# Kernel optimization log

Measured on AMD Instinct MI355X. Metric: run time of the kernel, lower is better.

The kernel has to match this reference:

```python
import jax, jax.numpy as jnp
import numpy as np

N_NODES = 8192
N_EDGES = 49152
IN_F, HID, H1, H2, OUT_F = 128, 64, 64, 5, 32
N_BONDS = 64


def setup_inputs() -> dict:
    key = jax.random.key(0)
    ks = jax.random.split(key, 12)
    s = 0.05
    return {
        "x": jax.random.normal(ks[0], (N_NODES, IN_F), jnp.float32),
        "edge_index": jax.random.randint(ks[1], (2, N_EDGES), 0, N_NODES, jnp.int32),
        "lefts": jax.random.randint(ks[2], (N_BONDS,), 0, N_NODES, jnp.int32),
        "rights": jax.random.randint(ks[3], (N_BONDS,), 0, N_NODES, jnp.int32),
        "W1": jax.random.normal(ks[4], (H1 * HID, IN_F), jnp.float32) * s,
        "att_src1": jax.random.normal(ks[5], (H1, HID), jnp.float32) * s,
        "att_dst1": jax.random.normal(ks[6], (H1, HID), jnp.float32) * s,
        "b1": jnp.zeros((H1 * HID,), jnp.float32),
        "W2": jax.random.normal(ks[7], (H2 * OUT_F, H1 * HID), jnp.float32) * s,
        "att_src2": jax.random.normal(ks[8], (H2, OUT_F), jnp.float32) * s,
        "att_dst2": jax.random.normal(ks[9], (H2, OUT_F), jnp.float32) * s,
        "b2": jnp.zeros((OUT_F,), jnp.float32),
    }


def _gat_conv(x, src, dst, W, a_src, a_dst, b, concat):
    # x: [N, F_in]; W: [H*C, F_in]; a_src/a_dst: [H, C]
    N = x.shape[0]
    H, C = a_src.shape
    h = (x @ W.T).reshape(N, H, C)                    # [N, H, C]
    alpha_s = jnp.einsum("nhc,hc->nh", h, a_src)      # [N, H]
    alpha_d = jnp.einsum("nhc,hc->nh", h, a_dst)
    logits = jax.nn.leaky_relu(alpha_s[src] + alpha_d[dst], negative_slope=0.2)  # [E, H]
    # scatter-softmax over incoming edges of each destination node
    m = jax.ops.segment_max(logits, dst, num_segments=N)
    e = jnp.exp(logits - m[dst])
    denom = jax.ops.segment_sum(e, dst, num_segments=N)
    alpha = e / denom[dst]                            # [E, H]
    msg = h[src] * alpha[:, :, None]                  # [E, H, C]
    out = jax.ops.segment_sum(msg, dst, num_segments=N)  # [N, H, C]
    out = out.reshape(N, H * C) if concat else out.mean(axis=1)
    return out + b


def reference(x, edge_index, lefts, rights, W1, att_src1, att_dst1, b1,
              W2, att_src2, att_dst2, b2):
    N = x.shape[0]
    loops = jnp.arange(N, dtype=edge_index.dtype)
    src = jnp.concatenate([edge_index[0], loops])
    dst = jnp.concatenate([edge_index[1], loops])
    x1 = jax.nn.elu(_gat_conv(x, src, dst, W1, att_src1, att_dst1, b1, concat=True))
    x2 = _gat_conv(x1, src, dst, W2, att_src2, att_dst2, b2, concat=False)  # [N, OUT_F]
    score = (x2[lefts] + x2[rights]).sum(axis=-1)     # [N_BONDS]
    return jax.nn.softmax(score, axis=0)
```

## Files before the change

kernel.cpp:

```cpp
#include <hip/hip_runtime.h>
#include <hip/hip_bf16.h>
#include <math.h>

#define N_NODES  8192
#define N_EDGES  49152
#define E_TOT    57344
#define IN_F     128
#define HID      64
#define NH1      64
#define NH2      5
#define OUT_F    32
#define F1       4096
#define F2       160
#define N_BONDS  64
#define ET       16
#define NP       4
#define HG       16

typedef short bf16x8 __attribute__((ext_vector_type(8)));
typedef float f32x4  __attribute__((ext_vector_type(4)));

__device__ __forceinline__ float lrelu(float x){ return x > 0.f ? x : 0.2f*x; }

__device__ __forceinline__ unsigned short bf16_rne(float f){
    unsigned u = __float_as_uint(f);
    unsigned r = u + 0x7FFF + ((u >> 16) & 1);
    return (unsigned short)(r >> 16);
}
__device__ __forceinline__ float bf16f(unsigned short h){
    return __uint_as_float((unsigned)h << 16);
}

__device__ __forceinline__ void block_sync_lds(){
    asm volatile("s_waitcnt lgkmcnt(0)" ::: "memory");
    __builtin_amdgcn_s_barrier();
    asm volatile("" ::: "memory");
}

__device__ __forceinline__ void gload_lds16(const unsigned short* gp, unsigned short* lp_base){
    __builtin_amdgcn_global_load_lds(
        (const __attribute__((address_space(1))) unsigned int*)(const void*)gp,
        (__attribute__((address_space(3))) unsigned int*)(void*)lp_base,
        16, 0, 0);
}

__global__ __launch_bounds__(256) void k_countprep(const int* __restrict__ ei,
        int* counts,
        const float* __restrict__ W1, const float* __restrict__ W2,
        const float* __restrict__ a_s, const float* __restrict__ a_d,
        unsigned short* __restrict__ w1fh, unsigned short* __restrict__ w1fl,
        unsigned short* __restrict__ w2fh, unsigned short* __restrict__ w2fl,
        float* __restrict__ vv){
    int b = blockIdx.x, t = threadIdx.x;
    if (b < 192){
        int i = b*256 + t;
        if (i < N_EDGES) atomicAdd(&counts[ei[N_EDGES + i]], 1);
    } else if (b < 448){
        int g = (b-192)*256 + t;
        int lane = g & 63, ct = (g >> 6) & 3, ks = (g >> 8) & 3, hg = g >> 10;
        int col = hg*64 + ct*16 + (lane & 15);
        int k = ks*32 + (lane >> 4)*8;
        const float* src = W1 + (size_t)col*IN_F + k;
        bf16x8 hv, lv;
        #pragma unroll
        for (int j=0;j<8;j++){
            float f = src[j];
            unsigned short hb = bf16_rne(f);
            hv[j] = (short)hb;
            lv[j] = (short)bf16_rne(f - bf16f(hb));
        }
        *(bf16x8*)(w1fh + (size_t)g*8) = hv;
        *(bf16x8*)(w1fl + (size_t)g*8) = lv;
    } else if (b < 768){
        int g = (b-448)*256 + t;
        int lane = g & 63, ni = (g >> 6) % 10, kc = g / 640;
        int n = ni*16 + (lane & 15);
        int k = kc*32 + (lane >> 4)*8;
        const float* src = W2 + (size_t)n*F1 + k;
        bf16x8 hv, lv;
        #pragma unroll
        for (int j=0;j<8;j++){
            float f = src[j];
            unsigned short hb = bf16_rne(f);
            hv[j] = (short)hb;
            lv[j] = (short)bf16_rne(f - bf16f(hb));
        }
        *(bf16x8*)(w2fh + (size_t)g*8) = hv;
        *(bf16x8*)(w2fl + (size_t)g*8) = lv;
    } else {
        int idx = (b-768)*256 + t;
        int j = idx >> 7, k = idx & 127;
        int h = j & 63;
        const float* ap = (j < 64) ? a_s : a_d;
        float s = 0.f;
        for (int c = 0; c < HID; c++)
            s += ap[h*HID + c] * W1[(size_t)(h*HID + c)*IN_F + k];
        vv[k*128 + j] = s;
    }
}

__global__ __launch_bounds__(1024) void k_scan(const int* __restrict__ counts,
                                               int* __restrict__ row_start,
                                               int* __restrict__ cursor){
    __shared__ int wsum[16];
    int t = threadIdx.x;
    int v[8]; int sum = 0;
    #pragma unroll
    for (int i=0;i<8;i++){ v[i] = counts[t*8+i] + 1; sum += v[i]; }
    int sc = sum;
    #pragma unroll
    for (int off=1; off<64; off<<=1){
        int up = __shfl_up(sc, off);
        if ((t & 63) >= off) sc += up;
    }
    int wid = t >> 6;
    if ((t & 63) == 63) wsum[wid] = sc;
    __syncthreads();
    if (t < 16){
        int ws = wsum[t];
        #pragma unroll
        for (int off=1; off<16; off<<=1){
            int up = __shfl_up(ws, off, 16);
            if (t >= off) ws += up;
        }
        wsum[t] = ws;
    }
    __syncthreads();
    int wbase = (wid == 0) ? 0 : wsum[wid-1];
    int run = wbase + sc - sum;
    #pragma unroll
    for (int i=0;i<8;i++){ row_start[t*8+i] = run; cursor[t*8+i] = run; run += v[i]; }
    if (t == 1023) row_start[N_NODES] = wsum[15];
}

__global__ __launch_bounds__(256) void k_fillalpha(const int* __restrict__ ei,
        int* cursor, int* __restrict__ csr_src,
        const float* __restrict__ x, const float* __restrict__ vv,
        float* __restrict__ as1, float* __restrict__ ad1){
    int b = blockIdx.x, t = threadIdx.x;
    if (b < 224){
        int i = b*256 + t;
        if (i >= E_TOT) return;
        int s, d;
        if (i < N_EDGES){ s = ei[i]; d = ei[N_EDGES + i]; }
        else { s = i - N_EDGES; d = s; }
        int pos = atomicAdd(&cursor[d], 1);
        csr_src[pos] = s;
    } else {
        __shared__ float xs[8][IN_F];
        int bb = b - 224;
        int nb = bb*8;
        {
            int r = t >> 5, c4 = t & 31;
            *(float4*)&xs[r][c4*4] = *(const float4*)(x + (size_t)(nb+r)*IN_F + c4*4);
        }
        __syncthreads();
        int half = t >> 7, tl = t & 127;
        int n0 = nb + half*4;
        float a0=0.f, a1=0.f, a2=0.f, a3=0.f;
        #pragma unroll 4
        for (int k=0;k<IN_F;k++){
            float v = vv[k*128 + tl];
            a0 += xs[half*4+0][k]*v; a1 += xs[half*4+1][k]*v;
            a2 += xs[half*4+2][k]*v; a3 += xs[half*4+3][k]*v;
        }
        int hd = tl & 63;
        float* outp = (tl < 64) ? as1 : ad1;
        outp[(n0+0)*NH1 + hd] = a0;
        outp[(n0+1)*NH1 + hd] = a1;
        outp[(n0+2)*NH1 + hd] = a2;
        outp[(n0+3)*NH1 + hd] = a3;
    }
}

__global__ __launch_bounds__(256) void k_aggx64(const float* __restrict__ x,
        const float* __restrict__ as1, const float* __restrict__ ad1,
        const int* __restrict__ row_start, const int* __restrict__ csr_src,
        unsigned short* __restrict__ txhi){
    int n = blockIdx.x, t = threadIdx.x;
    __shared__ float ad_s[NH1];
    __shared__ float wt[ET][NH1];
    __shared__ int   st[ET];
    __shared__ float xs[ET][IN_F];
    int e0 = row_start[n], e1 = row_start[n+1];
    if (t < NH1) ad_s[t] = ad1[n*NH1 + t];
    int hq = t >> 4, f0 = (t & 15)*8;
    float acc[4][8] = {};
    float D[4] = {0.f, 0.f, 0.f, 0.f};
    for (int eb = e0; eb < e1; eb += ET){
        int ne = min(ET, e1 - eb);
        if (t < ne) st[t] = csr_src[eb + t];
        __syncthreads();
        for (int idx = t; idx < ne*32; idx += 256){
            int e = idx >> 5, f4 = idx & 31;
            *(float4*)&xs[e][f4*4] = *(const float4*)(x + (size_t)st[e]*IN_F + f4*4);
        }
        for (int idx = t; idx < ne*NH1; idx += 256){
            int e = idx >> 6, hh = idx & 63;
            wt[e][hh] = __expf(lrelu(as1[st[e]*NH1 + hh] + ad_s[hh]));
        }
        __syncthreads();
        for (int e = 0; e < ne; e++){
            float4 v0 = *(const float4*)&xs[e][f0];
            float4 v1 = *(const float4*)&xs[e][f0+4];
            float xv[8] = {v0.x,v0.y,v0.z,v0.w,v1.x,v1.y,v1.z,v1.w};
            #pragma unroll
            for (int c=0;c<4;c++){
                float w = wt[e][hq*4 + c];
                D[c] += w;
                #pragma unroll
                for (int j=0;j<8;j++) acc[c][j] += w*xv[j];
            }
        }
        __syncthreads();
    }
    #pragma unroll
    for (int c=0;c<4;c++){
        float dinv = 1.f / D[c];
        bf16x8 hv;
        #pragma unroll
        for (int j=0;j<8;j++) hv[j] = (short)bf16_rne(acc[c][j] * dinv);
        size_t o = ((size_t)(hq*4 + c)*N_NODES + n)*IN_F + f0;
        *(bf16x8*)(txhi + o) = hv;
    }
}

__global__ __launch_bounds__(512, 4) void k_gemm12(
        const unsigned short* __restrict__ txhi,
        const unsigned short* __restrict__ w1fh, const unsigned short* __restrict__ w1fl,
        const unsigned short* __restrict__ w2fh, const unsigned short* __restrict__ w2fl,
        const float* __restrict__ b1,
        float* __restrict__ P){
    __shared__ __attribute__((aligned(16))) unsigned short Als[8192];
    __shared__ __attribute__((aligned(16))) unsigned short W1sh[8192];
    __shared__ __attribute__((aligned(16))) unsigned short W2s[20480];
    __shared__ __attribute__((aligned(16))) unsigned short X1s[4096];

    const int tid  = threadIdx.x;
    const int wave = tid >> 6, lane = tid & 63;
    const int wr = wave & 1, wc = wave >> 1;
    const int q = lane >> 4, l16 = lane & 15;
    const int row0 = blockIdx.x * 64;
    const int g = blockIdx.y;
    const int h0 = g * HG;
    const int nbase = (wc < 2) ? wc*3 : 6 + (wc-2)*2;

    {
        const unsigned short* Ab = txhi + ((size_t)h0*N_NODES + row0)*IN_F;
        const unsigned short* W1b = w1fh + (size_t)h0*8192;
        #pragma unroll
        for (int j=0;j<2;j++){
            int idx = j*8 + wave;
            int eo = idx*512 + lane*8;
            int row = eo >> 7;
            int se = (eo & ~127) | ((eo & 127) ^ ((row & 7) << 3));
            gload_lds16(Ab + se, &Als[idx*512]);
        }
        #pragma unroll
        for (int j=0;j<2;j++){
            int idx = j*8 + wave;
            gload_lds16(W1b + idx*512 + lane*8, &W1sh[idx*512]);
        }
    }

    f32x4 acc2[2][3] = {};
    bf16x8 wlo[4];

    #pragma unroll 1
    for (int hh = 0; hh < HG; hh++){
        const int h = h0 + hh;
        block_sync_lds();
        {
            const unsigned short* W1lb = w1fl + (size_t)h*8192;
            #pragma unroll
            for (int ks=0;ks<4;ks++)
                wlo[ks] = *(const bf16x8*)(W1lb + (size_t)(ks*4 + wc)*512 + lane*8);
        }
        asm volatile("" ::: "memory");
        {
            const unsigned short* W2bh = w2fh + (size_t)h*10240;
            const unsigned short* W2bl = w2fl + (size_t)h*10240;
            #pragma unroll
            for (int j=0;j<5;j++){
                int idx = j*8 + wave;
                const unsigned short* src = (idx < 20) ? (W2bh + idx*512 + lane*8)
                                                       : (W2bl + (idx-20)*512 + lane*8);
                gload_lds16(src, &W2s[idx*512]);
            }
        }
        asm volatile("s_waitcnt vmcnt(9)" ::: "memory");
        __builtin_amdgcn_s_barrier();
        f32x4 c1[2] = {};
        __builtin_amdgcn_s_setprio(1);
        #pragma unroll
        for (int ks=0;ks<4;ks++){
            bf16x8 bh = *(const bf16x8*)&W1sh[(ks*4 + wc)*512 + lane*8];
            #pragma unroll
            for (int mi=0;mi<2;mi++){
                int arow = wr*32 + mi*16 + l16;
                int sidx = (arow*128 + ks*32 + q*8) ^ ((arow & 7) << 3);
                bf16x8 af = *(const bf16x8*)&Als[sidx];
                c1[mi] = __builtin_amdgcn_mfma_f32_16x16x32_bf16(af, bh, c1[mi], 0,0,0);
                c1[mi] = __builtin_amdgcn_mfma_f32_16x16x32_bf16(af, wlo[ks], c1[mi], 0,0,0);
            }
        }
        __builtin_amdgcn_s_setprio(0);
        {
            int col = wc*16 + l16;
            float b = b1[h*64 + col];
            #pragma unroll
            for (int mi=0;mi<2;mi++){
                #pragma unroll
                for (int i=0;i<4;i++){
                    float v = c1[mi][i] + b;
                    float o = v > 0.f ? v : (__expf(v) - 1.f);
                    int row = wr*32 + mi*16 + q*4 + i;
                    int sidx = (row*64 + col) ^ ((row & 7) << 3);
                    X1s[sidx] = bf16_rne(o);
                }
            }
        }
        asm volatile("s_waitcnt vmcnt(0) lgkmcnt(0)" ::: "memory");
        __builtin_amdgcn_s_barrier();
        if (hh + 1 < HG){
            const unsigned short* Ab = txhi + ((size_t)(h+1)*N_NODES + row0)*IN_F;
            const unsigned short* W1b = w1fh + (size_t)(h+1)*8192;
            #pragma unroll
            for (int j=0;j<2;j++){
                int idx = j*8 + wave;
                int eo = idx*512 + lane*8;
                int row = eo >> 7;
                int se = (eo & ~127) | ((eo & 127) ^ ((row & 7) << 3));
                gload_lds16(Ab + se, &Als[idx*512]);
            }
            #pragma unroll
            for (int j=0;j<2;j++){
                int idx = j*8 + wave;
                gload_lds16(W1b + idx*512 + lane*8, &W1sh[idx*512]);
            }
        }
        __builtin_amdgcn_s_setprio(1);
        #pragma unroll
        for (int ks=0;ks<2;ks++){
            bf16x8 a2[2];
            #pragma unroll
            for (int mi=0;mi<2;mi++){
                int row = wr*32 + mi*16 + l16;
                int sidx = (row*64 + ks*32 + q*8) ^ ((row & 7) << 3);
                a2[mi] = *(const bf16x8*)&X1s[sidx];
            }
            if (wc < 2){
                #pragma unroll
                for (int ni=0;ni<3;ni++){
                    int f = (ks*10 + nbase + ni)*512 + lane*8;
                    bf16x8 bh = *(const bf16x8*)&W2s[f];
                    bf16x8 bl = *(const bf16x8*)&W2s[10240 + f];
                    #pragma unroll
                    for (int mi=0;mi<2;mi++){
                        acc2[mi][ni] = __builtin_amdgcn_mfma_f32_16x16x32_bf16(a2[mi], bh, acc2[mi][ni], 0,0,0);
                        acc2[mi][ni] = __builtin_amdgcn_mfma_f32_16x16x32_bf16(a2[mi], bl, acc2[mi][ni], 0,0,0);
                    }
                }
            } else {
                #pragma unroll
                for (int ni=0;ni<2;ni++){
                    int f = (ks*10 + nbase + ni)*512 + lane*8;
                    bf16x8 bh = *(const bf16x8*)&W2s[f];
                    bf16x8 bl = *(const bf16x8*)&W2s[10240 + f];
                    #pragma unroll
                    for (int mi=0;mi<2;mi++){
                        acc2[mi][ni] = __builtin_amdgcn_mfma_f32_16x16x32_bf16(a2[mi], bh, acc2[mi][ni], 0,0,0);
                        acc2[mi][ni] = __builtin_amdgcn_mfma_f32_16x16x32_bf16(a2[mi], bl, acc2[mi][ni], 0,0,0);
                    }
                }
            }
        }
        __builtin_amdgcn_s_setprio(0);
    }

    float* outp = P + ((size_t)g*N_NODES + row0)*F2;
    #pragma unroll
    for (int mi=0;mi<2;mi++)
        #pragma unroll
        for (int ni=0;ni<3;ni++){
            if (wc >= 2 && ni >= 2) continue;
            #pragma unroll
            for (int i=0;i<4;i++){
                int rr = wr*32 + mi*16 + q*4 + i;
                int cc = (nbase + ni)*16 + l16;
                outp[(size_t)rr*F2 + cc] = acc2[mi][ni][i];
            }
        }
}

__global__ __launch_bounds__(256) void k_redalpha(const float* __restrict__ P,
        const float* __restrict__ att_s, const float* __restrict__ att_d,
        float* __restrict__ h2, float* __restrict__ as2, float* __restrict__ ad2){
    __shared__ float hs[32][164];
    __shared__ float avs[160], avd[160];
    int b = blockIdx.x, t = threadIdx.x;
    int n0 = b*32;
    if (t < 160){ avs[t] = att_s[t]; avd[t] = att_d[t]; }
    const int NV = N_NODES*F2/4;
    int base = b * (32*F2/4);
    #pragma unroll
    for (int v=0; v<5; v++){
        int i = base + v*256 + t;
        float4 a = ((const float4*)P)[i];
        #pragma unroll
        for (int kb=1; kb<NP; kb++){
            float4 bb = ((const float4*)P)[(size_t)kb*NV + i];
            a.x+=bb.x; a.y+=bb.y; a.z+=bb.z; a.w+=bb.w;
        }
        ((float4*)h2)[i] = a;
        int flat = (v*256 + t)*4;
        int n = flat / F2, c = flat % F2;
        *(float4*)&hs[n][c] = a;
    }
    __syncthreads();
    if (t < 160){
        int n = t/5, hh = t%5;
        const float* hp = &hs[n][hh*32];
        const float* ap = &avs[hh*32];
        const float* dp = &avd[hh*32];
        float s=0.f, d=0.f;
        #pragma unroll
        for (int c=0;c<32;c++){ float hv=hp[c]; s += hv*ap[c]; d += hv*dp[c]; }
        as2[(n0+n)*NH2 + hh] = s;
        ad2[(n0+n)*NH2 + hh] = d;
    }
}

__global__ __launch_bounds__(192) void k_agg2(const float* __restrict__ h2,
        const float* __restrict__ as2, const float* __restrict__ ad2,
        const int* __restrict__ row_start, const int* __restrict__ csr_src,
        const float* __restrict__ b2, float* __restrict__ x2){
    int n = blockIdx.x, t = threadIdx.x;
    __shared__ float ad_s[NH2], sacc[F2];
    int e0 = row_start[n], e1 = row_start[n+1];
    if (t < NH2) ad_s[t] = ad2[n*NH2 + t];
    __syncthreads();
    if (t < F2){
        int h = t >> 5;
        float adh = ad_s[h];
        float acc = 0.f, D = 0.f;
        for (int e=e0;e<e1;e++){
            int s = csr_src[e];
            float w = __expf(lrelu(as2[s*NH2 + h] + adh));
            acc += w * h2[(size_t)s*F2 + t];
            D += w;
        }
        sacc[t] = acc / D;
    }
    __syncthreads();
    if (t < OUT_F){
        float v = (sacc[t] + sacc[t+32] + sacc[t+64] + sacc[t+96] + sacc[t+128]) * 0.2f + b2[t];
        x2[n*OUT_F + t] = v;
    }
}

__global__ __launch_bounds__(64) void k_bond(const float* __restrict__ x2,
        const int* __restrict__ lefts, const int* __restrict__ rights,
        float* __restrict__ out){
    int b = threadIdx.x;
    int L = lefts[b], R = rights[b];
    float s = 0.f;
    #pragma unroll
    for (int c=0;c<OUT_F;c+=4){
        float4 l4 = *(const float4*)(x2 + (size_t)L*OUT_F + c);
        float4 r4 = *(const float4*)(x2 + (size_t)R*OUT_F + c);
        s += l4.x+l4.y+l4.z+l4.w + r4.x+r4.y+r4.z+r4.w;
    }
    float m = s;
    #pragma unroll
    for (int off=1; off<64; off<<=1) m = fmaxf(m, __shfl_xor(m, off));
    float e = expf(s - m);
    float sum = e;
    #pragma unroll
    for (int off=1; off<64; off<<=1) sum += __shfl_xor(sum, off);
    out[b] = e / sum;
}

extern "C" void kernel_launch(void* const* d_in, const int* in_sizes, int n_in,
                              void* d_out, int out_size, void* d_ws, size_t ws_size,
                              hipStream_t stream){
    const float* x      = (const float*)d_in[0];
    const int*   ei     = (const int*)  d_in[1];
    const int*   lefts  = (const int*)  d_in[2];
    const int*   rights = (const int*)  d_in[3];
    const float* W1     = (const float*)d_in[4];
    const float* att_s1 = (const float*)d_in[5];
    const float* att_d1 = (const float*)d_in[6];
    const float* b1     = (const float*)d_in[7];
    const float* W2     = (const float*)d_in[8];
    const float* att_s2 = (const float*)d_in[9];
    const float* att_d2 = (const float*)d_in[10];
    const float* b2     = (const float*)d_in[11];
    float* out = (float*)d_out;

    char* ws = (char*)d_ws;
    size_t off = 0;
    auto alloc = [&](size_t bytes) -> void* {
        void* p = ws + off;
        off += (bytes + 255) & ~(size_t)255;
        return p;
    };
    unsigned short* txhi = (unsigned short*)alloc((size_t)NH1*N_NODES*IN_F*2);
    float* part   = (float*)alloc((size_t)NP*N_NODES*F2*4);
    float* h2     = (float*)alloc((size_t)N_NODES*F2*4);
    float* as1    = (float*)alloc((size_t)N_NODES*NH1*4);
    float* ad1    = (float*)alloc((size_t)N_NODES*NH1*4);
    float* as2    = (float*)alloc((size_t)N_NODES*NH2*4);
    float* ad2    = (float*)alloc((size_t)N_NODES*NH2*4);
    float* x2     = (float*)alloc((size_t)N_NODES*OUT_F*4);
    float* vv     = (float*)alloc((size_t)IN_F*128*4);
    unsigned short* w1fh = (unsigned short*)alloc((size_t)F1*IN_F*2);
    unsigned short* w1fl = (unsigned short*)alloc((size_t)F1*IN_F*2);
    unsigned short* w2fh = (unsigned short*)alloc((size_t)128*10*512*2);
    unsigned short* w2fl = (unsigned short*)alloc((size_t)128*10*512*2);
    int* counts    = (int*)alloc((size_t)N_NODES*4);
    int* row_start = (int*)alloc((size_t)(N_NODES+1)*4);
    int* cursor    = (int*)alloc((size_t)N_NODES*4);
    int* csr_src   = (int*)alloc((size_t)E_TOT*4);

    hipMemsetAsync(counts, 0, (size_t)N_NODES*4, stream);
    k_countprep<<<832, 256, 0, stream>>>(ei, counts, W1, W2, att_s1, att_d1,
                                         w1fh, w1fl, w2fh, w2fl, vv);
    k_scan<<<1, 1024, 0, stream>>>(counts, row_start, cursor);

    k_fillalpha<<<1248, 256, 0, stream>>>(ei, cursor, csr_src, x, vv, as1, ad1);

    k_aggx64<<<N_NODES, 256, 0, stream>>>(x, as1, ad1, row_start, csr_src, txhi);

    k_gemm12<<<dim3(128, NP), 512, 0, stream>>>(txhi, w1fh, w1fl, w2fh, w2fl, b1, part);
    k_redalpha<<<256, 256, 0, stream>>>(part, att_s2, att_d2, h2, as2, ad2);

    k_agg2<<<N_NODES, 192, 0, stream>>>(h2, as2, ad2, row_start, csr_src, b2, x2);

    k_bond<<<1, 64, 0, stream>>>(x2, lefts, rights, out);
}
```

Measured before the change: 210.3 us.

## Fuse count+scan into prep kernel and split-K reduction into GEMM tail

Edge-degree counting now runs in block 0 of the weight-prep kernel using an LDS histogram followed by an in-block scan. This removes the memset and the separate scan kernel. The layer-2 partial-sum reduction and alpha computation are moved into the GEMM kernel, where the last-arriving block per row tile (detected via an atomic counter) performs it. This eliminates two to three launches and their tail gaps, at the cost of a serial single-block histogram of 49K edges and extra fence/atomic work at the GEMM tail.

```diff
diff --git a/kernel.cpp b/kernel.cpp
--- a/kernel.cpp
+++ b/kernel.cpp
@@ -44,19 +44,52 @@
         16, 0, 0);
 }
 
-__global__ __launch_bounds__(256) void k_countprep(const int* __restrict__ ei,
-        int* counts,
+__global__ __launch_bounds__(512) void k_prepscan(const int* __restrict__ ei,
         const float* __restrict__ W1, const float* __restrict__ W2,
         const float* __restrict__ a_s, const float* __restrict__ a_d,
         unsigned short* __restrict__ w1fh, unsigned short* __restrict__ w1fl,
         unsigned short* __restrict__ w2fh, unsigned short* __restrict__ w2fl,
-        float* __restrict__ vv){
+        float* __restrict__ vv,
+        int* __restrict__ row_start, int* __restrict__ cursor,
+        int* __restrict__ rctr){
+    __shared__ int cnt[N_NODES];
+    __shared__ int wsum8[8];
     int b = blockIdx.x, t = threadIdx.x;
-    if (b < 192){
-        int i = b*256 + t;
-        if (i < N_EDGES) atomicAdd(&counts[ei[N_EDGES + i]], 1);
-    } else if (b < 448){
-        int g = (b-192)*256 + t;
+    if (b == 0){
+        for (int i = t; i < N_NODES; i += 512) cnt[i] = 0;
+        __syncthreads();
+        for (int i = t; i < N_EDGES; i += 512) atomicAdd(&cnt[ei[N_EDGES + i]], 1);
+        __syncthreads();
+        int v[16]; int sum = 0;
+        #pragma unroll
+        for (int k=0;k<16;k++){ v[k] = cnt[t*16+k] + 1; sum += v[k]; }
+        int sc = sum;
+        #pragma unroll
+        for (int off=1; off<64; off<<=1){
+            int up = __shfl_up(sc, off);
+            if ((t & 63) >= off) sc += up;
+        }
+        int wid = t >> 6;
+        if ((t & 63) == 63) wsum8[wid] = sc;
+        __syncthreads();
+        if (t < 8){
+            int ws = wsum8[t];
+            #pragma unroll
+            for (int off=1; off<8; off<<=1){
+                int up = __shfl_up(ws, off, 8);
+                if (t >= off) ws += up;
+            }
+            wsum8[t] = ws;
+        }
+        __syncthreads();
+        int wbase = (wid == 0) ? 0 : wsum8[wid-1];
+        int run = wbase + sc - sum;
+        #pragma unroll
+        for (int k=0;k<16;k++){ row_start[t*16+k] = run; cursor[t*16+k] = run; run += v[k]; }
+        if (t == 511) row_start[N_NODES] = wsum8[7];
+        if (t < 128) rctr[t] = 0;
+    } else if (b < 129){
+        int g = (b-1)*512 + t;
         int lane = g & 63, ct = (g >> 6) & 3, ks = (g >> 8) & 3, hg = g >> 10;
         int col = hg*64 + ct*16 + (lane & 15);
         int k = ks*32 + (lane >> 4)*8;
@@ -71,8 +104,8 @@
         }
         *(bf16x8*)(w1fh + (size_t)g*8) = hv;
         *(bf16x8*)(w1fl + (size_t)g*8) = lv;
-    } else if (b < 768){
-        int g = (b-448)*256 + t;
+    } else if (b < 289){
+        int g = (b-129)*512 + t;
         int lane = g & 63, ni = (g >> 6) % 10, kc = g / 640;
         int n = ni*16 + (lane & 15);
         int k = kc*32 + (lane >> 4)*8;
@@ -88,7 +121,7 @@
         *(bf16x8*)(w2fh + (size_t)g*8) = hv;
         *(bf16x8*)(w2fl + (size_t)g*8) = lv;
     } else {
-        int idx = (b-768)*256 + t;
+        int idx = (b-289)*512 + t;
         int j = idx >> 7, k = idx & 127;
         int h = j & 63;
         const float* ap = (j < 64) ? a_s : a_d;
@@ -97,40 +130,6 @@
             s += ap[h*HID + c] * W1[(size_t)(h*HID + c)*IN_F + k];
         vv[k*128 + j] = s;
     }
-}
-
-__global__ __launch_bounds__(1024) void k_scan(const int* __restrict__ counts,
-                                               int* __restrict__ row_start,
-                                               int* __restrict__ cursor){
-    __shared__ int wsum[16];
-    int t = threadIdx.x;
-    int v[8]; int sum = 0;
-    #pragma unroll
-    for (int i=0;i<8;i++){ v[i] = counts[t*8+i] + 1; sum += v[i]; }
-    int sc = sum;
-    #pragma unroll
-    for (int off=1; off<64; off<<=1){
-        int up = __shfl_up(sc, off);
-        if ((t & 63) >= off) sc += up;
-    }
-    int wid = t >> 6;
-    if ((t & 63) == 63) wsum[wid] = sc;
-    __syncthreads();
-    if (t < 16){
-        int ws = wsum[t];
-        #pragma unroll
-        for (int off=1; off<16; off<<=1){
-            int up = __shfl_up(ws, off, 16);
-            if (t >= off) ws += up;
-        }
-        wsum[t] = ws;
-    }
-    __syncthreads();
-    int wbase = (wid == 0) ? 0 : wsum[wid-1];
-    int run = wbase + sc - sum;
-    #pragma unroll
-    for (int i=0;i<8;i++){ row_start[t*8+i] = run; cursor[t*8+i] = run; run += v[i]; }
-    if (t == 1023) row_start[N_NODES] = wsum[15];
 }
 
 __global__ __launch_bounds__(256) void k_fillalpha(const int* __restrict__ ei,
@@ -230,11 +229,15 @@
         const unsigned short* __restrict__ w1fh, const unsigned short* __restrict__ w1fl,
         const unsigned short* __restrict__ w2fh, const unsigned short* __restrict__ w2fl,
         const float* __restrict__ b1,
-        float* __restrict__ P){
-    __shared__ __attribute__((aligned(16))) unsigned short Als[8192];
-    __shared__ __attribute__((aligned(16))) unsigned short W1sh[8192];
-    __shared__ __attribute__((aligned(16))) unsigned short W2s[20480];
-    __shared__ __attribute__((aligned(16))) unsigned short X1s[4096];
+        float* __restrict__ P,
+        const float* __restrict__ att_s2, const float* __restrict__ att_d2,
+        float* __restrict__ h2, float* __restrict__ as2, float* __restrict__ ad2,
+        int* __restrict__ rctr){
+    __shared__ __attribute__((aligned(16))) char smem_[81920];
+    unsigned short* Als  = (unsigned short*)smem_;
+    unsigned short* W1sh = (unsigned short*)(smem_ + 16384);
+    unsigned short* W2s  = (unsigned short*)(smem_ + 32768);
+    unsigned short* X1s  = (unsigned short*)(smem_ + 73728);
 
     const int tid  = threadIdx.x;
     const int wave = tid >> 6, lane = tid & 63;
@@ -391,43 +394,45 @@
                 outp[(size_t)rr*F2 + cc] = acc2[mi][ni][i];
             }
         }
-}
-
-__global__ __launch_bounds__(256) void k_redalpha(const float* __restrict__ P,
-        const float* __restrict__ att_s, const float* __restrict__ att_d,
-        float* __restrict__ h2, float* __restrict__ as2, float* __restrict__ ad2){
-    __shared__ float hs[32][164];
-    __shared__ float avs[160], avd[160];
-    int b = blockIdx.x, t = threadIdx.x;
-    int n0 = b*32;
-    if (t < 160){ avs[t] = att_s[t]; avd[t] = att_d[t]; }
-    const int NV = N_NODES*F2/4;
-    int base = b * (32*F2/4);
-    #pragma unroll
-    for (int v=0; v<5; v++){
-        int i = base + v*256 + t;
-        float4 a = ((const float4*)P)[i];
-        #pragma unroll
-        for (int kb=1; kb<NP; kb++){
-            float4 bb = ((const float4*)P)[(size_t)kb*NV + i];
-            a.x+=bb.x; a.y+=bb.y; a.z+=bb.z; a.w+=bb.w;
-        }
-        ((float4*)h2)[i] = a;
-        int flat = (v*256 + t)*4;
-        int n = flat / F2, c = flat % F2;
-        *(float4*)&hs[n][c] = a;
-    }
+
+    __threadfence();
     __syncthreads();
-    if (t < 160){
-        int n = t/5, hh = t%5;
-        const float* hp = &hs[n][hh*32];
-        const float* ap = &avs[hh*32];
-        const float* dp = &avd[hh*32];
-        float s=0.f, d=0.f;
-        #pragma unroll
-        for (int c=0;c<32;c++){ float hv=hp[c]; s += hv*ap[c]; d += hv*dp[c]; }
-        as2[(n0+n)*NH2 + hh] = s;
-        ad2[(n0+n)*NH2 + hh] = d;
+    volatile int* sdp = (volatile int*)(smem_ + 73728);
+    if (tid == 0) *sdp = atomicAdd(&rctr[blockIdx.x], 1);
+    __syncthreads();
+    int done = *sdp;
+    if (done == NP-1){
+        __threadfence();
+        const int NV4 = N_NODES*F2/4;
+        const float4* P4 = (const float4*)P;
+        float4* h24 = (float4*)h2;
+        float* hsf = (float*)smem_;
+        #pragma unroll
+        for (int v=0; v<5; v++){
+            int li = v*512 + tid;
+            int i = row0*40 + li;
+            float4 a = P4[i];
+            #pragma unroll
+            for (int g2=1; g2<NP; g2++){
+                float4 b = P4[(size_t)g2*NV4 + i];
+                a.x+=b.x; a.y+=b.y; a.z+=b.z; a.w+=b.w;
+            }
+            h24[i] = a;
+            int n = li/40, c4 = li%40;
+            *(float4*)&hsf[n*164 + c4*4] = a;
+        }
+        __syncthreads();
+        if (tid < 320){
+            int n = tid/5, hh = tid%5;
+            const float* hp = &hsf[n*164 + hh*32];
+            const float* ap = att_s2 + hh*32;
+            const float* dp = att_d2 + hh*32;
+            float s=0.f, d=0.f;
+            #pragma unroll
+            for (int c=0;c<32;c++){ float hv=hp[c]; s += hv*ap[c]; d += hv*dp[c]; }
+            as2[(row0+n)*NH2 + hh] = s;
+            ad2[(row0+n)*NH2 + hh] = d;
+        }
     }
 }
 
@@ -518,22 +523,21 @@
     unsigned short* w1fl = (unsigned short*)alloc((size_t)F1*IN_F*2);
     unsigned short* w2fh = (unsigned short*)alloc((size_t)128*10*512*2);
     unsigned short* w2fl = (unsigned short*)alloc((size_t)128*10*512*2);
-    int* counts    = (int*)alloc((size_t)N_NODES*4);
     int* row_start = (int*)alloc((size_t)(N_NODES+1)*4);
     int* cursor    = (int*)alloc((size_t)N_NODES*4);
     int* csr_src   = (int*)alloc((size_t)E_TOT*4);
-
-    hipMemsetAsync(counts, 0, (size_t)N_NODES*4, stream);
-    k_countprep<<<832, 256, 0, stream>>>(ei, counts, W1, W2, att_s1, att_d1,
-                                         w1fh, w1fl, w2fh, w2fl, vv);
-    k_scan<<<1, 1024, 0, stream>>>(counts, row_start, cursor);
+    int* rctr      = (int*)alloc((size_t)128*4);
+
+    k_prepscan<<<321, 512, 0, stream>>>(ei, W1, W2, att_s1, att_d1,
+                                        w1fh, w1fl, w2fh, w2fl, vv,
+                                        row_start, cursor, rctr);
 
     k_fillalpha<<<1248, 256, 0, stream>>>(ei, cursor, csr_src, x, vv, as1, ad1);
 
     k_aggx64<<<N_NODES, 256, 0, stream>>>(x, as1, ad1, row_start, csr_src, txhi);
 
-    k_gemm12<<<dim3(128, NP), 512, 0, stream>>>(txhi, w1fh, w1fl, w2fh, w2fl, b1, part);
-    k_redalpha<<<256, 256, 0, stream>>>(part, att_s2, att_d2, h2, as2, ad2);
+    k_gemm12<<<dim3(128, NP), 512, 0, stream>>>(txhi, w1fh, w1fl, w2fh, w2fl, b1,
+                                                part, att_s2, att_d2, h2, as2, ad2, rctr);
 
     k_agg2<<<N_NODES, 192, 0, stream>>>(h2, as2, ad2, row_start, csr_src, b2, x2);
 
```

Result: slower. 361.6 us (+72.0%).
